# Performance work log

Measured on AMD Instinct MI355X. Metric: run time of the kernel, lower is better.

## Reference

```python
import jax, jax.numpy as jnp
import numpy as np

B, NPTS, NBASIS, DIM, H, CH = 8, 1024, 8, 8, 512, 16
EPSILON = 1000.0
P = 2
VOLUME = 2.0 ** DIM  # MC domain [-1,1]^dim


def setup_inputs() -> dict:
    key = jax.random.key(0)
    ks = jax.random.split(key, 10)
    s = jax.random.uniform(ks[0], (NPTS, DIM), dtype=jnp.float32) * 2.0 - 1.0  # MC samples in [-1,1]^dim
    x = jax.random.uniform(ks[1], (1, DIM), dtype=jnp.float32) * 2.0 - 1.0     # eval point
    Wfirst = jax.random.normal(ks[2], (DIM, H), dtype=jnp.float32) / np.sqrt(DIM)
    bfirst = jax.random.normal(ks[3], (H,), dtype=jnp.float32) * 0.01
    Wb = jax.random.normal(ks[4], (NBASIS, H, H), dtype=jnp.float32) / np.sqrt(H)
    bb = jax.random.normal(ks[5], (NBASIS, H), dtype=jnp.float32) * 0.01
    Wlast = jax.random.normal(ks[6], (H, CH), dtype=jnp.float32) / np.sqrt(H)
    blast = jax.random.normal(ks[7], (CH,), dtype=jnp.float32) * 0.01
    Wf = jax.random.normal(ks[8], (DIM, CH), dtype=jnp.float32) / np.sqrt(DIM)
    bf = jax.random.normal(ks[9], (CH,), dtype=jnp.float32) * 0.01
    return dict(s=s, x=x, Wfirst=Wfirst, bfirst=bfirst, Wb=Wb, bb=bb,
                Wlast=Wlast, blast=blast, Wf=Wf, bf=bf)


def _basis_all(pts, Wfirst, bfirst, Wb, bb, Wlast, blast):
    # pts: [M, DIM] -> all n basis nets, batch-repeated: [NBASIS, B, M, CH]
    a0 = jax.nn.elu(jnp.einsum('md,dh->mh', pts, Wfirst) + bfirst)          # [M, H]
    a0 = jnp.broadcast_to(a0[None], (B,) + a0.shape)                         # [B, M, H] (repeat over batch)
    a1 = jax.nn.elu(jnp.einsum('bmh,ihk->ibmk', a0, Wb) + bb[:, None, None, :])  # [n, B, M, H]
    return jnp.einsum('ibmk,kc->ibmc', a1, Wlast) + blast                    # [n, B, M, CH]


def reference(s, x, Wfirst, bfirst, Wb, bb, Wlast, blast, Wf, bf):
    # func(s): linear map realizing the projected function  [NPTS, CH]
    f_s = jnp.einsum('nd,dc->nc', s, Wf) + bf
    basis_s = _basis_all(s, Wfirst, bfirst, Wb, bb, Wlast, blast)            # [n, B, NPTS, CH]
    diff = f_s[None, None] - basis_s                                          # broadcast over n, B
    # Monte Carlo integral of (func - basis_i)^p over [-1,1]^dim, per channel
    integral = VOLUME * jnp.mean(diff ** P, axis=-2)                          # [n, B, CH]
    norm_pc = integral ** (1.0 / P)                                           # Lp norm per channel
    norm_b = jnp.sum(jnp.abs(norm_pc) ** P, axis=-1, keepdims=True) ** (1.0 / P)  # [n, B, 1]
    mu = jnp.where(norm_b <= EPSILON, norm_b, 0.0)                            # [n, B, 1]
    basis_x = _basis_all(x, Wfirst, bfirst, Wb, bb, Wlast, blast)[:, :, 0, :]  # [n, B, CH]
    out = jnp.sum(mu * basis_x, axis=0)                                       # [B, CH]
    normalization = 1e-7 + jnp.sum(mu, axis=0)                                # [B, 1]
    return out / normalization
```

## Files before the change

### kernel.cpp

```cpp
#include <hip/hip_runtime.h>

typedef _Float16 half8 __attribute__((ext_vector_type(8)));
typedef float f32x4 __attribute__((ext_vector_type(4)));
typedef float f32x16 __attribute__((ext_vector_type(16)));
typedef unsigned int u32x4 __attribute__((ext_vector_type(4)));

#define NPTS 1024
#define NB 8
#define HDIM 512
#define CH 16
#define RT 1088

#define OFF_WBF 0u
#define OFF_A0F (4u*1024u*1024u)
#define A0SZ    (64u*RT*16u)
#define OFF_WLF (OFF_A0F + A0SZ)
#define OFF_FS  (OFF_WLF + 16384u)
#define OFF_PP  (OFF_FS + 65536u)
#define PPSZ    (32u*RT*16u*4u)
#define OFF_IS  (OFF_PP + PPSZ)
#define OFF_BX  (OFF_IS + 64u)

__device__ __forceinline__ float elu(float z) { return z > 0.f ? z : expm1f(z); }

__device__ __forceinline__ void gl16(const void* g, void* l) {
  __builtin_amdgcn_global_load_lds(
      (const __attribute__((address_space(1))) unsigned int*)g,
      (__attribute__((address_space(3))) unsigned int*)l, 16, 0, 0);
}

__global__ __launch_bounds__(256) void kPrep(const float* __restrict__ s,
    const float* __restrict__ x, const float* __restrict__ Wfirst,
    const float* __restrict__ bfirst, const float* __restrict__ Wb,
    const float* __restrict__ Wlast, const float* __restrict__ Wf,
    const float* __restrict__ bf,
    _Float16* __restrict__ Wbf, _Float16* __restrict__ Wlf,
    _Float16* __restrict__ a0f, float* __restrict__ f_s,
    float* __restrict__ Isum) {
  __shared__ __align__(16) float sm[8192];
  int b = blockIdx.x, t = threadIdx.x;
  if (b < 1024) {
    int i = b >> 7, koct = (b >> 1) & 63, n = (b & 1) * 256 + t;
    const float* src = Wb + ((size_t)i * 512 + koct * 8) * 512 + n;
    float v[8];
#pragma unroll
    for (int j = 0; j < 8; ++j) v[j] = src[j * 512];
    union { _Float16 h[8]; u32x4 u; } hu;
#pragma unroll
    for (int j = 0; j < 8; ++j) hu.h[j] = (_Float16)v[j];
    *(u32x4*)(Wbf + ((size_t)(i * 64 + koct) * 512 + n) * 8) = hu.u;
  } else if (b < 1296) {
    int rr = t >> 6, tl = t & 63;
    int m = (b - 1024) * 4 + rr;
    float* sv = &sm[rr * 8];
    if (tl < 8) sv[tl] = (m < 1024) ? s[m * 8 + tl] : (m == 1024 ? x[tl] : 0.f);
    __syncthreads();
    size_t o = ((size_t)tl * RT + m) * 8;
    if (m <= 1024) {
      float acc[8];
#pragma unroll
      for (int jj = 0; jj < 8; ++jj) acc[jj] = bfirst[8 * tl + jj];
#pragma unroll
      for (int d = 0; d < 8; ++d) {
        float sd = sv[d];
        f32x4 w0 = *(const f32x4*)&Wfirst[d * 512 + 8 * tl];
        f32x4 w1 = *(const f32x4*)&Wfirst[d * 512 + 8 * tl + 4];
#pragma unroll
        for (int e = 0; e < 4; ++e) { acc[e] += sd * w0[e]; acc[4 + e] += sd * w1[e]; }
      }
      union { _Float16 h[8]; u32x4 u; } hu;
#pragma unroll
      for (int jj = 0; jj < 8; ++jj) hu.h[jj] = (_Float16)elu(acc[jj]);
      *(u32x4*)(a0f + o) = hu.u;
      if (m < 1024 && tl < 16) {
        float a = bf[tl];
#pragma unroll
        for (int d = 0; d < 8; ++d) a += sv[d] * Wf[d * 16 + tl];
        f_s[m * 16 + tl] = a;
      }
    } else {
      u32x4 z;
#pragma unroll
      for (int e = 0; e < 4; ++e) z[e] = 0u;
      *(u32x4*)(a0f + o) = z;
    }
  } else {
    if (t < 8) Isum[t] = 0.f;
#pragma unroll
    for (int it = 0; it < 32; ++it) sm[t + 256 * it] = Wlast[t + 256 * it];
    __syncthreads();
#pragma unroll
    for (int p = 0; p < 4; ++p) {
      int oi = p * 256 + t;
      int ko = oi >> 4, ch = oi & 15;
      union { _Float16 h[8]; u32x4 u; } hu;
#pragma unroll
      for (int jj = 0; jj < 8; ++jj) hu.h[jj] = (_Float16)sm[(ko * 8 + jj) * 16 + ch];
      *(u32x4*)(Wlf + oi * 8) = hu.u;
    }
  }
}


#define STAGE(buf, ks) do {                                                          \
    int kb_ = (ks) * 8;                                                              \
    char* lA_ = lds + (buf) * 8192;                                                  \
    char* lB_ = lds + 16384 + (buf) * 16384;                                         \
    gl16(&a4[(size_t)(kb_ + (t >> 6)) * RT + m0 + (t & 63)], lA_ + t * 16);          \
    gl16(&a4[(size_t)(kb_ + 4 + (t >> 6)) * RT + m0 + (t & 63)], lA_ + 4096 + t * 16); \
    gl16(&b4[(size_t)(ib + kb_ + (t >> 7)) * 512 + n0 + (t & 127)], lB_ + t * 16);   \
    gl16(&b4[(size_t)(ib + kb_ + 2 + (t >> 7)) * 512 + n0 + (t & 127)], lB_ + 4096 + t * 16); \
    gl16(&b4[(size_t)(ib + kb_ + 4 + (t >> 7)) * 512 + n0 + (t & 127)], lB_ + 8192 + t * 16); \
    gl16(&b4[(size_t)(ib + kb_ + 6 + (t >> 7)) * 512 + n0 + (t & 127)], lB_ + 12288 + t * 16); \
  } while (0)

#define COMP(buf) do {                                                               \
    const u32x4* Ab_ = (const u32x4*)(lds + (buf) * 8192);                           \
    const u32x4* Bb_ = (const u32x4*)(lds + 16384 + (buf) * 16384);                  \
    _Pragma("unroll")                                                                \
    for (int kk = 0; kk < 4; ++kk) {                                                 \
      int ko_ = 2 * kk + q;                                                          \
      u32x4 av = Ab_[ko_ * 64 + wr * 32 + ln];                                       \
      u32x4 bv0 = Bb_[ko_ * 128 + nc + ln];                                          \
      u32x4 bv1 = Bb_[ko_ * 128 + nc + 32 + ln];                                     \
      acc0 = __builtin_amdgcn_mfma_f32_32x32x16_f16(                                 \
          __builtin_bit_cast(half8, av), __builtin_bit_cast(half8, bv0), acc0, 0, 0, 0); \
      acc1 = __builtin_amdgcn_mfma_f32_32x32x16_f16(                                 \
          __builtin_bit_cast(half8, av), __builtin_bit_cast(half8, bv1), acc1, 0, 0, 0); \
    }                                                                                \
  } while (0)

__global__ __launch_bounds__(256, 3) void kB(const _Float16* __restrict__ Wbf,
    const _Float16* __restrict__ a0f, const _Float16* __restrict__ Wlf,
    const float* __restrict__ bb, float* __restrict__ Pp) {
  __shared__ __align__(16) char lds[49152];
  int t = threadIdx.x, b = blockIdx.x;
  int i = b & 7, r = b >> 3;
  int nq = r & 3, mt = r >> 2;
  int m0 = mt * 64, n0 = nq * 128;
  int w = t >> 6, lane = t & 63, ln = lane & 31, q = lane >> 5;
  int wr = w & 1, nc = (w >> 1) * 64;
  int ib = i * 64;
  const u32x4* a4 = (const u32x4*)a0f;
  const u32x4* b4 = (const u32x4*)Wbf;

  f32x16 acc0, acc1;
#pragma unroll
  for (int rr = 0; rr < 16; ++rr) { acc0[rr] = 0.f; acc1[rr] = 0.f; }

  STAGE(0, 0);
  __syncthreads();
#pragma unroll
  for (int s = 0; s < 8; ++s) {
    if (s < 7) STAGE((s + 1) & 1, s + 1);
    COMP(s & 1);
    __syncthreads();
  }

  float* S2f = (float*)(lds + 16384);
#pragma unroll
  for (int z = 0; z < 4; ++z) S2f[t + 256 * z] = 0.f;

  _Float16* scr = (_Float16*)(lds + w * 4096);
  float bcA = bb[(size_t)i * 512 + n0 + nc + ln];
  float bcB = bb[(size_t)i * 512 + n0 + nc + 32 + ln];
#pragma unroll
  for (int rr = 0; rr < 16; ++rr) {
    int row = (rr & 3) + 8 * (rr >> 2) + 4 * q;
    float aA = elu(acc0[rr] + bcA);
    float aB = elu(acc1[rr] + bcB);
    int mt2 = row >> 4, m16 = row & 15;
    scr[(mt2 * 128 + (ln >> 3) * 16 + m16) * 8 + (ln & 7)] = (_Float16)aA;
    scr[(mt2 * 128 + (4 + (ln >> 3)) * 16 + m16) * 8 + (ln & 7)] = (_Float16)aB;
  }
  __syncthreads();

  const u32x4* s4 = (const u32x4*)(lds + w * 4096);
  const u32x4* w4 = (const u32x4*)Wlf;
  int ch = lane & 15, q4 = lane >> 4;
  int hb = (n0 + nc) >> 3;
  half8 wv0 = __builtin_bit_cast(half8, w4[(size_t)(hb + q4) * 16 + ch]);
  half8 wv1 = __builtin_bit_cast(half8, w4[(size_t)(hb + 4 + q4) * 16 + ch]);
#pragma unroll
  for (int mt2 = 0; mt2 < 2; ++mt2) {
    f32x4 D;
#pragma unroll
    for (int rr = 0; rr < 4; ++rr) D[rr] = 0.f;
    half8 p0 = __builtin_bit_cast(half8, s4[mt2 * 128 + q4 * 16 + ch]);
    half8 p1 = __builtin_bit_cast(half8, s4[mt2 * 128 + (4 + q4) * 16 + ch]);
    D = __builtin_amdgcn_mfma_f32_16x16x32_f16(p0, wv0, D, 0, 0, 0);
    D = __builtin_amdgcn_mfma_f32_16x16x32_f16(p1, wv1, D, 0, 0, 0);
#pragma unroll
    for (int rr = 0; rr < 4; ++rr)
      atomicAdd(&S2f[(wr * 32 + mt2 * 16 + q4 * 4 + rr) * 16 + ch], D[rr]);
  }
  __syncthreads();
  for (int o = t; o < 1024; o += 256) {
    int m = o >> 4, c2 = o & 15;
    Pp[((size_t)(i * 4 + nq) * RT + m0 + m) * 16 + c2] = S2f[m * 16 + c2];
  }
}

__global__ __launch_bounds__(256) void kRed(const float* __restrict__ Pp,
    const float* __restrict__ f_s, const float* __restrict__ blast,
    float* __restrict__ Isum, float* __restrict__ basisx) {
  __shared__ float wsum[4];
  int b = blockIdx.x, t = threadIdx.x;
  int i = b / 33, mt = b - i * 33;
  const float* P0 = Pp + (size_t)(i * 4) * RT * 16;
  const size_t PS = (size_t)RT * 16;
  if (mt == 32) {
    if (t < 16) {
      size_t o = (size_t)1024 * 16 + t;
      basisx[i * 16 + t] = P0[o] + P0[PS + o] + P0[2 * PS + o] + P0[3 * PS + o] + blast[t];
    }
    return;
  }
  float loc = 0.f;
#pragma unroll
  for (int p = 0; p < 2; ++p) {
    int item = t + p * 256;
    int m = mt * 32 + (item >> 4), ch = item & 15;
    size_t o = (size_t)m * 16 + ch;
    float bs = P0[o] + P0[PS + o] + P0[2 * PS + o] + P0[3 * PS + o] + blast[ch];
    float d = f_s[o] - bs;
    loc += d * d;
  }
  loc += __shfl_xor(loc, 1, 64);
  loc += __shfl_xor(loc, 2, 64);
  loc += __shfl_xor(loc, 4, 64);
  loc += __shfl_xor(loc, 8, 64);
  loc += __shfl_xor(loc, 16, 64);
  loc += __shfl_xor(loc, 32, 64);
  int lane = t & 63, w = t >> 6;
  if (lane == 0) wsum[w] = loc;
  __syncthreads();
  if (t == 0) atomicAdd(&Isum[i], wsum[0] + wsum[1] + wsum[2] + wsum[3]);
}

__global__ __launch_bounds__(128) void kFin(const float* __restrict__ Isum,
    const float* __restrict__ basisx, float* __restrict__ out) {
  __shared__ float muL[8];
  int t = threadIdx.x;
  if (t < 8) {
    float nb = 0.5f * sqrtf(Isum[t]);
    muL[t] = (nb <= 1000.0f) ? nb : 0.f;
  }
  __syncthreads();
  int ch = t & 15;
  float num = 0.f, den = 1e-7f;
#pragma unroll
  for (int i = 0; i < NB; ++i) {
    num += muL[i] * basisx[i * 16 + ch];
    den += muL[i];
  }
  out[t] = num / den;
}

extern "C" void kernel_launch(void* const* d_in, const int* in_sizes, int n_in,
                              void* d_out, int out_size, void* d_ws, size_t ws_size,
                              hipStream_t stream) {
  const float* s      = (const float*)d_in[0];
  const float* x      = (const float*)d_in[1];
  const float* Wfirst = (const float*)d_in[2];
  const float* bfirst = (const float*)d_in[3];
  const float* Wb     = (const float*)d_in[4];
  const float* bb     = (const float*)d_in[5];
  const float* Wlast  = (const float*)d_in[6];
  const float* blast  = (const float*)d_in[7];
  const float* Wf     = (const float*)d_in[8];
  const float* bf     = (const float*)d_in[9];

  char* ws = (char*)d_ws;
  _Float16* Wbf = (_Float16*)(ws + OFF_WBF);
  _Float16* a0f = (_Float16*)(ws + OFF_A0F);
  _Float16* Wlf = (_Float16*)(ws + OFF_WLF);
  float* f_s    = (float*)(ws + OFF_FS);
  float* Pp     = (float*)(ws + OFF_PP);
  float* Isum   = (float*)(ws + OFF_IS);
  float* basisx = (float*)(ws + OFF_BX);
  float* out    = (float*)d_out;

  kPrep<<<1297, 256, 0, stream>>>(s, x, Wfirst, bfirst, Wb, Wlast, Wf, bf,
                                  Wbf, Wlf, a0f, f_s, Isum);
  kB<<<544, 256, 0, stream>>>(Wbf, a0f, Wlf, bb, Pp);
  kRed<<<264, 256, 0, stream>>>(Pp, f_s, blast, Isum, basisx);
  kFin<<<1, 128, 0, stream>>>(Isum, basisx, out);
}
```

Baseline: 110.0 us.

## Fuse four kernels into one cooperative persistent kernel with grid syncs

Replaces the four separate launches (prep, GEMM, reduction, finalize) with a single cooperative kernel of 544 blocks that runs each stage as a device job separated by grid-wide barriers. Prep jobs are strided over the 544 blocks. The aim is to remove kernel launch gaps and per-launch overhead. In exchange it adds grid.sync costs and leaves many blocks idle in the later stages. If the cooperative launch fails, the code falls back to the original four-kernel path.

```diff
diff --git a/kernel.cpp b/kernel.cpp
--- a/kernel.cpp
+++ b/kernel.cpp
@@ -1,4 +1,7 @@
 #include <hip/hip_runtime.h>
+#include <hip/hip_cooperative_groups.h>
+
+namespace cg = cooperative_groups;
 
 typedef _Float16 half8 __attribute__((ext_vector_type(8)));
 typedef float f32x4 __attribute__((ext_vector_type(4)));
@@ -29,16 +32,15 @@
       (__attribute__((address_space(3))) unsigned int*)l, 16, 0, 0);
 }
 
-__global__ __launch_bounds__(256) void kPrep(const float* __restrict__ s,
-    const float* __restrict__ x, const float* __restrict__ Wfirst,
-    const float* __restrict__ bfirst, const float* __restrict__ Wb,
-    const float* __restrict__ Wlast, const float* __restrict__ Wf,
-    const float* __restrict__ bf,
+
+__device__ __forceinline__ void prep_job(int b, int t, float* sm,
+    const float* __restrict__ s, const float* __restrict__ x,
+    const float* __restrict__ Wfirst, const float* __restrict__ bfirst,
+    const float* __restrict__ Wb, const float* __restrict__ Wlast,
+    const float* __restrict__ Wf, const float* __restrict__ bf,
     _Float16* __restrict__ Wbf, _Float16* __restrict__ Wlf,
     _Float16* __restrict__ a0f, float* __restrict__ f_s,
     float* __restrict__ Isum) {
-  __shared__ __align__(16) float sm[8192];
-  int b = blockIdx.x, t = threadIdx.x;
   if (b < 1024) {
     int i = b >> 7, koct = (b >> 1) & 63, n = (b & 1) * 256 + t;
     const float* src = Wb + ((size_t)i * 512 + koct * 8) * 512 + n;
@@ -130,11 +132,10 @@
     }                                                                                \
   } while (0)
 
-__global__ __launch_bounds__(256, 3) void kB(const _Float16* __restrict__ Wbf,
-    const _Float16* __restrict__ a0f, const _Float16* __restrict__ Wlf,
-    const float* __restrict__ bb, float* __restrict__ Pp) {
-  __shared__ __align__(16) char lds[49152];
-  int t = threadIdx.x, b = blockIdx.x;
+__device__ __forceinline__ void gemm_job(int b, int t, char* lds,
+    const _Float16* __restrict__ Wbf, const _Float16* __restrict__ a0f,
+    const _Float16* __restrict__ Wlf, const float* __restrict__ bb,
+    float* __restrict__ Pp) {
   int i = b & 7, r = b >> 3;
   int nq = r & 3, mt = r >> 2;
   int m0 = mt * 64, n0 = nq * 128;
@@ -151,9 +152,9 @@
   STAGE(0, 0);
   __syncthreads();
 #pragma unroll
-  for (int s = 0; s < 8; ++s) {
-    if (s < 7) STAGE((s + 1) & 1, s + 1);
-    COMP(s & 1);
+  for (int st = 0; st < 8; ++st) {
+    if (st < 7) STAGE((st + 1) & 1, st + 1);
+    COMP(st & 1);
     __syncthreads();
   }
 
@@ -201,11 +202,10 @@
   }
 }
 
-__global__ __launch_bounds__(256) void kRed(const float* __restrict__ Pp,
-    const float* __restrict__ f_s, const float* __restrict__ blast,
-    float* __restrict__ Isum, float* __restrict__ basisx) {
-  __shared__ float wsum[4];
-  int b = blockIdx.x, t = threadIdx.x;
+__device__ __forceinline__ void red_job(int b, int t, float* wsum,
+    const float* __restrict__ Pp, const float* __restrict__ f_s,
+    const float* __restrict__ blast, float* __restrict__ Isum,
+    float* __restrict__ basisx) {
   int i = b / 33, mt = b - i * 33;
   const float* P0 = Pp + (size_t)(i * 4) * RT * 16;
   const size_t PS = (size_t)RT * 16;
@@ -238,23 +238,87 @@
   if (t == 0) atomicAdd(&Isum[i], wsum[0] + wsum[1] + wsum[2] + wsum[3]);
 }
 
+__device__ __forceinline__ void fin_job(int t, float* muL,
+    const float* __restrict__ Isum, const float* __restrict__ basisx,
+    float* __restrict__ out) {
+  if (t < 8) {
+    float nb = 0.5f * sqrtf(Isum[t]);
+    muL[t] = (nb <= 1000.0f) ? nb : 0.f;
+  }
+  __syncthreads();
+  if (t < 128) {
+    int ch = t & 15;
+    float num = 0.f, den = 1e-7f;
+#pragma unroll
+    for (int i = 0; i < NB; ++i) {
+      num += muL[i] * basisx[i * 16 + ch];
+      den += muL[i];
+    }
+    out[t] = num / den;
+  }
+}
+
+__global__ __launch_bounds__(256, 3) void kFused(
+    const float* __restrict__ s, const float* __restrict__ x,
+    const float* __restrict__ Wfirst, const float* __restrict__ bfirst,
+    const float* __restrict__ Wb, const float* __restrict__ bb,
+    const float* __restrict__ Wlast, const float* __restrict__ blast,
+    const float* __restrict__ Wf, const float* __restrict__ bf,
+    _Float16* __restrict__ Wbf, _Float16* __restrict__ Wlf,
+    _Float16* __restrict__ a0f, float* __restrict__ f_s, float* __restrict__ Pp,
+    float* __restrict__ Isum, float* __restrict__ basisx, float* __restrict__ out) {
+  __shared__ __align__(16) char lds[49152];
+  cg::grid_group grid = cg::this_grid();
+  int t = threadIdx.x;
+
+  for (int job = blockIdx.x; job < 1297; job += 544) {
+    prep_job(job, t, (float*)lds, s, x, Wfirst, bfirst, Wb, Wlast, Wf, bf,
+             Wbf, Wlf, a0f, f_s, Isum);
+    __syncthreads();
+  }
+  grid.sync();
+
+  gemm_job(blockIdx.x, t, lds, Wbf, a0f, Wlf, bb, Pp);
+  grid.sync();
+
+  if (blockIdx.x < 264)
+    red_job(blockIdx.x, t, (float*)lds, Pp, f_s, blast, Isum, basisx);
+  grid.sync();
+
+  if (blockIdx.x == 0) fin_job(t, (float*)lds, Isum, basisx, out);
+}
+
+__global__ __launch_bounds__(256) void kPrep(const float* __restrict__ s,
+    const float* __restrict__ x, const float* __restrict__ Wfirst,
+    const float* __restrict__ bfirst, const float* __restrict__ Wb,
+    const float* __restrict__ Wlast, const float* __restrict__ Wf,
+    const float* __restrict__ bf,
+    _Float16* __restrict__ Wbf, _Float16* __restrict__ Wlf,
+    _Float16* __restrict__ a0f, float* __restrict__ f_s,
+    float* __restrict__ Isum) {
+  __shared__ __align__(16) float sm[8192];
+  prep_job(blockIdx.x, threadIdx.x, sm, s, x, Wfirst, bfirst, Wb, Wlast, Wf, bf,
+           Wbf, Wlf, a0f, f_s, Isum);
+}
+
+__global__ __launch_bounds__(256, 3) void kB(const _Float16* __restrict__ Wbf,
+    const _Float16* __restrict__ a0f, const _Float16* __restrict__ Wlf,
+    const float* __restrict__ bb, float* __restrict__ Pp) {
+  __shared__ __align__(16) char lds[49152];
+  gemm_job(blockIdx.x, threadIdx.x, lds, Wbf, a0f, Wlf, bb, Pp);
+}
+
+__global__ __launch_bounds__(256) void kRed(const float* __restrict__ Pp,
+    const float* __restrict__ f_s, const float* __restrict__ blast,
+    float* __restrict__ Isum, float* __restrict__ basisx) {
+  __shared__ float wsum[4];
+  red_job(blockIdx.x, threadIdx.x, wsum, Pp, f_s, blast, Isum, basisx);
+}
+
 __global__ __launch_bounds__(128) void kFin(const float* __restrict__ Isum,
     const float* __restrict__ basisx, float* __restrict__ out) {
   __shared__ float muL[8];
-  int t = threadIdx.x;
-  if (t < 8) {
-    float nb = 0.5f * sqrtf(Isum[t]);
-    muL[t] = (nb <= 1000.0f) ? nb : 0.f;
-  }
-  __syncthreads();
-  int ch = t & 15;
-  float num = 0.f, den = 1e-7f;
-#pragma unroll
-  for (int i = 0; i < NB; ++i) {
-    num += muL[i] * basisx[i * 16 + ch];
-    den += muL[i];
-  }
-  out[t] = num / den;
+  fin_job(threadIdx.x, muL, Isum, basisx, out);
 }
 
 extern "C" void kernel_launch(void* const* d_in, const int* in_sizes, int n_in,
@@ -281,9 +345,15 @@
   float* basisx = (float*)(ws + OFF_BX);
   float* out    = (float*)d_out;
 
-  kPrep<<<1297, 256, 0, stream>>>(s, x, Wfirst, bfirst, Wb, Wlast, Wf, bf,
-                                  Wbf, Wlf, a0f, f_s, Isum);
-  kB<<<544, 256, 0, stream>>>(Wbf, a0f, Wlf, bb, Pp);
-  kRed<<<264, 256, 0, stream>>>(Pp, f_s, blast, Isum, basisx);
-  kFin<<<1, 128, 0, stream>>>(Isum, basisx, out);
-}
+  void* args[] = {&s, &x, &Wfirst, &bfirst, &Wb, &bb, &Wlast, &blast, &Wf, &bf,
+                  &Wbf, &Wlf, &a0f, &f_s, &Pp, &Isum, &basisx, &out};
+  hipError_t e = hipLaunchCooperativeKernel((const void*)kFused, dim3(544),
+                                            dim3(256), args, 0, stream);
+  if (e != hipSuccess) {
+    kPrep<<<1297, 256, 0, stream>>>(s, x, Wfirst, bfirst, Wb, Wlast, Wf, bf,
+                                    Wbf, Wlf, a0f, f_s, Isum);
+    kB<<<544, 256, 0, stream>>>(Wbf, a0f, Wlf, bb, Pp);
+    kRed<<<264, 256, 0, stream>>>(Pp, f_s, blast, Isum, basisx);
+    kFin<<<1, 128, 0, stream>>>(Isum, basisx, out);
+  }
+}
```

After: 313.8 us. 185% more time.
